# Performance work log

Measured on AMD Instinct MI355X. Metric: run time of the kernel, lower is better.

The kernel has to match this reference:

```python
import jax, jax.numpy as jnp
import numpy as np
from jax import lax

N_SAMPLES = 2 ** 15          # 32768
N_FRAMES = 128
N_HARMONICS = 8
FILT_SIZE = 64
N_EVENTS = 8
N_SCALE = 128                # len(MusicalScale()) assumed = 128 (MIDI notes)
NYQ = 11025.0                # SR22050 nyquist
MIN_F0 = 40.0 / NYQ
MAX_F0 = 3000.0 / NYQ
F0_SPAN = MAX_F0 - MIN_F0
MIN_RES = 0.9
RES_SPAN = 1.0 - MIN_RES
PI = float(np.pi)

# packed layout slices (order of param_sizes dict)
SL_F0 = slice(0, 128)
SL_FINE = slice(128, 256)
SL_AMP = slice(256, 384)
SL_HAMP = slice(384, 392)
SL_HDEC = slice(392, 400)
SL_FENV = slice(400, 464)


def lin_interp(x, out_size):
    """F.interpolate(mode='linear', align_corners=False) along last axis."""
    n = x.shape[-1]
    pos = (jnp.arange(out_size, dtype=x.dtype) + 0.5) * (n / out_size) - 0.5
    pos = jnp.clip(pos, 0.0, n - 1)
    lo = jnp.floor(pos).astype(jnp.int32)
    hi = jnp.minimum(lo + 1, n - 1)
    w = pos - lo.astype(x.dtype)
    return x[..., lo] * (1.0 - w) + x[..., hi] * w


def setup_inputs() -> dict:
    key = jax.random.key(0)
    k1, k2 = jax.random.split(key)
    B = 32 * N_EVENTS  # 256 event rows
    packed = jax.random.normal(k1, (B, 464), dtype=jnp.float32)
    # musical scale: MIDI-note center frequencies normalized by nyquist
    midi = np.arange(N_SCALE)
    freqs = 440.0 * 2.0 ** ((midi - 69) / 12.0) / NYQ
    frequencies = jnp.asarray(freqs, dtype=jnp.float32)
    noise = jax.random.uniform(k2, (B, 1, N_SAMPLES), dtype=jnp.float32)  # mapped to (-1,1) in reference
    return {"packed": packed, "frequencies": frequencies, "noise": noise}


def reference(packed, frequencies, noise):
    B = packed.shape[0]
    p = jax.nn.sigmoid(packed)  # Model applies activation(p) before SynthParams

    # f0: softmax over discrete scale bins, weighted sum of normalized freqs
    f0w = jax.nn.softmax(p[:, SL_F0], axis=-1)             # [B, 128]
    f0 = (f0w @ frequencies)[:, None, None]                # [B,1,1]
    f0 = jnp.broadcast_to(f0, (B, 1, N_FRAMES))            # repeat over frames
    f0 = f0 * NYQ
    f0 = MIN_F0 + f0 * F0_SPAN                             # [B,1,128]
    # NOTE: source computes `f0 + f0 + f0_fine` and discards it -> f0_fine unused

    harmonic_factors = jnp.arange(1, N_HARMONICS + 1, dtype=p.dtype)
    osc = f0 * harmonic_factors[None, :, None]             # [B,8,128]
    radians = osc / NYQ * PI
    radians = lin_interp(radians, N_SAMPLES)               # [B,8,32768]
    osc_bank = jnp.sin(jnp.cumsum(radians, axis=-1))

    harm_decay = MIN_RES + p[:, SL_HDEC] * RES_SPAN        # [B,8]
    harm_amp = p[:, SL_HAMP]                               # [B,8]
    amp = p[:, SL_AMP][:, None, :] * 2.0 - 1.0             # [B,1,128]
    amp_full = lin_interp(amp, N_SAMPLES)                  # [B,1,32768]

    noise_filter = p[:, SL_FENV][:, None, :]               # [B,1,64]
    noise_filter = lin_interp(noise_filter, N_SAMPLES // 2)
    noise_filter = jnp.pad(noise_filter, ((0, 0), (0, 0), (0, 1)))  # [B,1,16385]

    noise_u = noise * 2.0 - 1.0                            # uniform(-1,1)
    noise_spec = jnp.fft.rfft(noise_u, axis=-1, norm='ortho')
    filt = jnp.fft.irfft(noise_spec * noise_filter, n=N_SAMPLES, axis=-1, norm='ortho')
    filt = filt * jnp.clip(amp_full, 0.0, 1.0)             # [B,1,32768]

    # leaky-accumulator recurrence over frames
    def step(cur, a_i):  # cur [B,8], a_i [B]
        cur = jnp.clip(cur + a_i[:, None] * harm_amp, 0.0, 1.0)
        out = cur
        cur = cur * harm_decay
        return cur, out

    amp_t = amp[:, 0, :].T                                 # [128, B]
    _, outs = lax.scan(step, jnp.zeros((B, N_HARMONICS), dtype=p.dtype), amp_t)
    x = jnp.transpose(outs, (1, 2, 0))                     # [B,8,128]
    x = jnp.where(x >= PI, 0.0, x)
    x = lin_interp(x, N_SAMPLES)                           # [B,8,32768]
    x = x * osc_bank
    x = filt + x
    x = x.reshape(-1, N_EVENTS, N_HARMONICS, N_SAMPLES)
    x = jnp.sum(x, axis=(1, 2))[:, None, :]                # [batch,1,32768]
    return x
```

## Files before the change

kernel.cpp:

```cpp
#include <hip/hip_runtime.h>
#include <math.h>

#ifndef M_PI
#define M_PI 3.14159265358979323846
#endif

#define NSAMP 32768
#define MHALF 16384
#define TWO_PI_F 6.2831853071795864f
#define PSTRIDE 1089

__device__ __forceinline__ double dsig(double x) { return 1.0 / (1.0 + exp(-x)); }

__global__ __launch_bounds__(128) void prep_kernel(
    const float* __restrict__ packed, const float* __restrict__ freqs,
    unsigned long long* __restrict__ step, float* __restrict__ env,
    float* __restrict__ amp, float* __restrict__ fenv)
{
    int b = blockIdx.x;
    int t = threadIdx.x;
    const float* pk = packed + b * 464;
    __shared__ double sh_num[128];
    __shared__ double sh_den[128];
    __shared__ double amp_d[128];

    double e_t = exp(dsig((double)pk[t]));
    sh_den[t] = e_t;
    sh_num[t] = e_t * (double)freqs[t];

    double av = dsig((double)pk[256 + t]) * 2.0 - 1.0;
    amp_d[t] = av;
    amp[b * 128 + t] = (float)av;

    if (t < 64) fenv[b * 64 + t] = (float)dsig((double)pk[400 + t]);
    __syncthreads();

    for (int off = 64; off > 0; off >>= 1) {
        if (t < off) { sh_den[t] += sh_den[t + off]; sh_num[t] += sh_num[t + off]; }
        __syncthreads();
    }

    if (t < 8) {
        const double NYQ = 11025.0;
        const double MIN_F0 = 40.0 / NYQ;
        const double MAX_F0 = 3000.0 / NYQ;
        const double F0_SPAN = MAX_F0 - MIN_F0;
        double f0 = sh_num[0] / sh_den[0];
        double F = f0 * NYQ;
        double G = MIN_F0 + F * F0_SPAN;
        double oscf = G * (double)(t + 1);
        double r = oscf / NYQ * M_PI;
        double rv = r / (2.0 * M_PI);
        rv -= floor(rv);
        step[b * 8 + t] = (unsigned long long)(rv * 18446744073709551616.0);

        double ha = dsig((double)pk[384 + t]);
        double hd = 0.9 + dsig((double)pk[392 + t]) * (1.0 - 0.9);
        double cur = 0.0;
        float* eo = env + (size_t)(b * 8 + t) * 128;
        for (int fr = 0; fr < 128; fr++) {
            cur = cur + amp_d[fr] * ha;
            cur = fmin(fmax(cur, 0.0), 1.0);
            eo[fr] = (float)cur;
            cur *= hd;
        }
    }
}

__device__ __forceinline__ float2 cmul(float2 a, float2 b) {
    return make_float2(a.x * b.x - a.y * b.y, a.x * b.y + a.y * b.x);
}

template<int INV>
__device__ __forceinline__ void fft4(float2& x0, float2& x1, float2& x2, float2& x3) {
    float2 s02 = make_float2(x0.x + x2.x, x0.y + x2.y);
    float2 d02 = make_float2(x0.x - x2.x, x0.y - x2.y);
    float2 s13 = make_float2(x1.x + x3.x, x1.y + x3.y);
    float2 d13 = make_float2(x1.x - x3.x, x1.y - x3.y);
    float2 j13 = INV ? make_float2(-d13.y, d13.x) : make_float2(d13.y, -d13.x);
    x0 = make_float2(s02.x + s13.x, s02.y + s13.y);
    x2 = make_float2(s02.x - s13.x, s02.y - s13.y);
    x1 = make_float2(d02.x + j13.x, d02.y + j13.y);
    x3 = make_float2(d02.x - j13.x, d02.y - j13.y);
}

#define V16(v, c) v[((((c) & 3) << 2) | ((c) >> 2))]

template<int INV>
__device__ __forceinline__ void fft16(float2 v[16]) {
    const float s = INV ? 1.0f : -1.0f;
#pragma unroll
    for (int b = 0; b < 4; b++) fft4<INV>(v[b], v[4 + b], v[8 + b], v[12 + b]);
    v[5]  = cmul(v[5],  make_float2(0.9238795325f,  s * 0.3826834324f));
    v[9]  = cmul(v[9],  make_float2(0.7071067812f,  s * 0.7071067812f));
    v[13] = cmul(v[13], make_float2(0.3826834324f,  s * 0.9238795325f));
    v[6]  = cmul(v[6],  make_float2(0.7071067812f,  s * 0.7071067812f));
    v[10] = cmul(v[10], make_float2(0.0f,           s * 1.0f));
    v[14] = cmul(v[14], make_float2(-0.7071067812f, s * 0.7071067812f));
    v[7]  = cmul(v[7],  make_float2(0.3826834324f,  s * 0.9238795325f));
    v[11] = cmul(v[11], make_float2(-0.7071067812f, s * 0.7071067812f));
    v[15] = cmul(v[15], make_float2(-0.9238795325f, s * -0.3826834324f));
#pragma unroll
    for (int p = 0; p < 4; p++) fft4<INV>(v[4 * p], v[4 * p + 1], v[4 * p + 2], v[4 * p + 3]);
}

__device__ __forceinline__ int zaddr(int k) {
    int p = k & 15, k2 = k >> 4;
    int s = 256 * (k2 & 3) + 16 * ((k2 >> 2) & 15) + (k2 >> 6);
    return p * PSTRIDE + s + (s >> 4);
}

__device__ __forceinline__ void plane_fwd(float2* __restrict__ Zp, int l) {
    {
        float sn, cs;
        __sincosf(TWO_PI_F * (float)l * (1.f / 1024.f), &sn, &cs);
        float2 w1 = make_float2(cs, -sn);
        const float2 jstep = make_float2(0.9238795325f, -0.3826834324f);
#pragma unroll
        for (int j = 0; j < 4; j++) {
            const int r = 64 * j + l;
            float2 u0 = Zp[r], u1 = Zp[256 + r], u2 = Zp[512 + r], u3 = Zp[768 + r];
            fft4<0>(u0, u1, u2, u3);
            float2 w2 = cmul(w1, w1);
            float2 w3 = cmul(w2, w1);
            Zp[r] = u0;
            Zp[256 + r] = cmul(u1, w1);
            Zp[512 + r] = cmul(u2, w2);
            Zp[768 + r] = cmul(u3, w3);
            w1 = cmul(w1, jstep);
        }
    }
    {
        const int k4 = l >> 4, c = l & 15;
        const int nbase = 256 * k4 + c;
        float sn, cs;
        __sincosf(TWO_PI_F * (float)c * (1.f / 256.f), &sn, &cs);
        const float2 wc = make_float2(cs, -sn);
        float2 v[16];
#pragma unroll
        for (int b = 0; b < 16; b++) v[b] = Zp[nbase + 16 * b];
        fft16<0>(v);
        const int pbase = 272 * k4 + c;
        Zp[pbase] = V16(v, 0);
        float2 w = wc;
#pragma unroll
        for (int kb = 1; kb < 16; kb++) {
            Zp[pbase + 17 * kb] = cmul(V16(v, kb), w);
            w = cmul(w, wc);
        }
    }
    {
        const int pbase = 272 * (l >> 4) + 17 * (l & 15);
        float2 v[16];
#pragma unroll
        for (int c = 0; c < 16; c++) v[c] = Zp[pbase + c];
        fft16<0>(v);
#pragma unroll
        for (int kc = 0; kc < 16; kc++) Zp[pbase + kc] = V16(v, kc);
    }
}

__device__ __forceinline__ void plane_inv(float2* __restrict__ Zp, int l) {
    {
        const int kb = l & 15;
        const int pbase = 272 * (l >> 4) + 17 * kb;
        float sn, cs;
        __sincosf(TWO_PI_F * (float)kb * (1.f / 256.f), &sn, &cs);
        const float2 wkb = make_float2(cs, sn);
        float2 v[16];
#pragma unroll
        for (int kc = 0; kc < 16; kc++) v[kc] = Zp[pbase + kc];
        fft16<1>(v);
        Zp[pbase] = V16(v, 0);
        float2 w = wkb;
#pragma unroll
        for (int nc = 1; nc < 16; nc++) {
            Zp[pbase + nc] = cmul(V16(v, nc), w);
            w = cmul(w, wkb);
        }
    }
    {
        const int k4 = l >> 4, nc = l & 15;
        const int pbase = 272 * k4 + nc;
        float sni, csi;
        __sincosf(TWO_PI_F * (float)(nc * k4) * (1.f / 1024.f), &sni, &csi);
        float2 t = make_float2(csi, sni);
        float sns, css;
        __sincosf(TWO_PI_F * (float)k4 * (1.f / 64.f), &sns, &css);
        const float2 st = make_float2(css, sns);
        float2 v[16];
#pragma unroll
        for (int kb = 0; kb < 16; kb++) v[kb] = Zp[pbase + 17 * kb];
        fft16<1>(v);
#pragma unroll
        for (int nb = 0; nb < 16; nb++) {
            Zp[pbase + 17 * nb] = cmul(V16(v, nb), t);
            t = cmul(t, st);
        }
    }
#pragma unroll
    for (int j = 0; j < 4; j++) {
        const int r = 64 * j + l;
        const int rp = r + (r >> 4);
        float2 u0 = Zp[rp], u1 = Zp[272 + rp], u2 = Zp[544 + rp], u3 = Zp[816 + rp];
        fft4<1>(u0, u1, u2, u3);
        Zp[rp] = u0; Zp[272 + rp] = u1; Zp[544 + rp] = u2; Zp[816 + rp] = u3;
    }
}

__device__ __forceinline__ float hinterp64(const float* f, int j) {
    float pos = ((float)j + 0.5f) * (1.0f / 256.0f) - 0.5f;
    pos = fminf(fmaxf(pos, 0.0f), 63.0f);
    int lo = (int)pos;
    int hi = min(lo + 1, 63);
    float w = pos - (float)lo;
    return f[lo] * (1.0f - w) + f[hi] * w;
}

__global__ __launch_bounds__(1024, 4) void fft_kernel(
    const float* __restrict__ noise, const float* __restrict__ amp,
    const float* __restrict__ fenv, float* __restrict__ filt)
{
    __shared__ float2 Z[16 * PSTRIDE];
    __shared__ float fenv_s[64];
    __shared__ float amp_s[128];
    const int bb = blockIdx.x;
    const int tid = threadIdx.x;
    const int wv = tid >> 6, l = tid & 63;

    if (tid < 64) fenv_s[tid] = fenv[bb * 64 + tid];
    if (tid < 128) amp_s[tid] = amp[bb * 128 + tid];

    const float2* nz = (const float2*)(noise + (size_t)bb * NSAMP);

    {
        float2 v[16];
#pragma unroll
        for (int a = 0; a < 16; a++) {
            float2 t = nz[a * 1024 + tid];
            v[a] = make_float2(t.x * 2.f - 1.f, t.y * 2.f - 1.f);
        }
        fft16<0>(v);
        float sn, cs;
        __sincosf(TWO_PI_F * (float)tid * (1.f / 16384.f), &sn, &cs);
        const float2 ws = make_float2(cs, -sn);
        Z[tid] = V16(v, 0);
        float2 w = ws;
#pragma unroll
        for (int k1 = 1; k1 < 16; k1++) {
            Z[k1 * PSTRIDE + tid] = cmul(V16(v, k1), w);
            w = cmul(w, ws);
        }
    }
    __syncthreads();

    plane_fwd(Z + wv * PSTRIDE, l);
    __syncthreads();

    const float invM = 1.0f / (float)MHALF;
    {
        float sn0, cs0;
        __sincosf((float)M_PI * (float)tid * (1.f / 16384.f), &sn0, &cs0);
        float2 t = make_float2(cs0, sn0);
        const float2 tstep = make_float2(0.98078528040323f, 0.19509032201613f);
        for (int k = tid; k <= 8192; k += 1024) {
            if (k == 0) {
                int i0 = zaddr(0);
                float2 Z0 = Z[i0];
                float Y0 = (Z0.x + Z0.y) * hinterp64(fenv_s, 0);
                float vv = Y0 * 0.5f * invM;
                Z[i0] = make_float2(vv, vv);
            } else if (k == 8192) {
                int i8 = zaddr(8192);
                float s = hinterp64(fenv_s, 8192) * invM;
                float2 Zk = Z[i8];
                Z[i8] = make_float2(Zk.x * s, Zk.y * s);
            } else {
                int ik = zaddr(k), imk = zaddr(16384 - k);
                float2 Zk = Z[ik], Zm = Z[imk];
                float Ex = 0.5f * (Zk.x + Zm.x);
                float Ey = 0.5f * (Zk.y - Zm.y);
                float Ox = 0.5f * (Zk.y + Zm.y);
                float Oy = -0.5f * (Zk.x - Zm.x);
                float cs = t.x, sn = t.y;
                float Xkx = Ex + cs * Ox + sn * Oy;
                float Xky = Ey + cs * Oy - sn * Ox;
                float Xmx = Ex - cs * Ox - sn * Oy;
                float Xmy = -Ey + cs * Oy - sn * Ox;
                float Hk = hinterp64(fenv_s, k);
                float Hm = hinterp64(fenv_s, 16384 - k);
                float Ykx = Xkx * Hk, Yky = Xky * Hk;
                float Ymx = Xmx * Hm, Ymy = Xmy * Hm;
                float Er = 0.5f * (Ykx + Ymx);
                float Ei = 0.5f * (Yky - Ymy);
                float Pr = 0.5f * (Ykx - Ymx);
                float Pi = 0.5f * (Yky + Ymy);
                float Oyx = Pr * cs - Pi * sn;
                float Oyy = Pr * sn + Pi * cs;
                Z[ik]  = make_float2((Er - Oyy) * invM, (Ei + Oyx) * invM);
                Z[imk] = make_float2((Er + Oyy) * invM, (-Ei + Oyx) * invM);
            }
            t = cmul(t, tstep);
        }
    }
    __syncthreads();

    plane_inv(Z + wv * PSTRIDE, l);
    __syncthreads();

    {
        const int tp = tid + (tid >> 4);
        float2 v[16];
#pragma unroll
        for (int k1 = 0; k1 < 16; k1++) v[k1] = Z[k1 * PSTRIDE + tp];
        float sn, cs;
        __sincosf(TWO_PI_F * (float)tid * (1.f / 16384.f), &sn, &cs);
        const float2 wg = make_float2(cs, sn);
        float2 w = wg;
#pragma unroll
        for (int k1 = 1; k1 < 16; k1++) {
            v[k1] = cmul(v[k1], w);
            w = cmul(w, wg);
        }
        fft16<1>(v);

        float2* fo = (float2*)(filt + (size_t)bb * NSAMP);
#pragma unroll
        for (int m = 0; m < 16; m++) {
            float2 y = V16(v, m);
            int A = m * 1024 + tid;
            int s0 = 2 * A;
            float p0 = ((float)s0 + 0.5f) * (1.0f / 256.0f) - 0.5f;
            float p1 = p0 + (1.0f / 256.0f);
            p0 = fminf(fmaxf(p0, 0.0f), 127.0f);
            p1 = fminf(fmaxf(p1, 0.0f), 127.0f);
            int l0 = (int)p0, l1 = (int)p1;
            int h0 = min(l0 + 1, 127), h1 = min(l1 + 1, 127);
            float w0a = p0 - (float)l0, w1a = p1 - (float)l1;
            float a0 = amp_s[l0] * (1.0f - w0a) + amp_s[h0] * w0a;
            float a1 = amp_s[l1] * (1.0f - w1a) + amp_s[h1] * w1a;
            a0 = fminf(fmaxf(a0, 0.0f), 1.0f);
            a1 = fminf(fmaxf(a1, 0.0f), 1.0f);
            fo[A] = make_float2(y.x * a0, y.y * a1);
        }
    }
}

__global__ __launch_bounds__(256) void synth_kernel(
    const unsigned long long* __restrict__ step, const float* __restrict__ env,
    const float* __restrict__ filt, float* __restrict__ out)
{
    const int chunk = blockIdx.x;
    const int g = blockIdx.y;
    const int tid = threadIdx.x;
    __shared__ float env_s[64 * 128];
    __shared__ unsigned long long step_s[64];

    const float* eg = env + (size_t)g * 64 * 128;
    for (int i = tid; i < 64 * 128; i += 256) env_s[i] = eg[i];
    if (tid < 64) step_s[tid] = step[g * 64 + tid];
    __syncthreads();

    const int s0 = chunk * 1024 + tid * 4;

    float4 aF = make_float4(0.f, 0.f, 0.f, 0.f);
#pragma unroll
    for (int e = 0; e < 8; e++) {
        const float4 f = *(const float4*)(filt + ((size_t)(g * 8 + e)) * NSAMP + s0);
        aF.x += f.x; aF.y += f.y; aF.z += f.z; aF.w += f.w;
    }

    float c0v[4], c1v[4], c2v[4];
    int lo0;
    {
        float pos0 = ((float)s0 + 0.5f) * (1.0f / 256.0f) - 0.5f;
        pos0 = fminf(fmaxf(pos0, 0.0f), 127.0f);
        lo0 = (int)pos0;
#pragma unroll
        for (int k = 0; k < 4; k++) {
            float pos = ((float)(s0 + k) + 0.5f) * (1.0f / 256.0f) - 0.5f;
            pos = fminf(fmaxf(pos, 0.0f), 127.0f);
            int lo = (int)pos;
            float w = pos - (float)lo;
            if (lo == lo0) { c0v[k] = 1.0f - w; c1v[k] = w;        c2v[k] = 0.0f; }
            else           { c0v[k] = 0.0f;     c1v[k] = 1.0f - w; c2v[k] = w;    }
        }
    }
    const int i1 = min(lo0 + 1, 127);
    int lo3b = lo0;
    {
        float pos = ((float)(s0 + 3) + 0.5f) * (1.0f / 256.0f) - 0.5f;
        pos = fminf(fmaxf(pos, 0.0f), 127.0f);
        lo3b = (int)pos;
    }
    const int i2 = min(lo3b + 1, 127);

    float a0 = 0.f, a1 = 0.f, a2 = 0.f, a3 = 0.f;
    const unsigned long long n0 = (unsigned long long)(unsigned)(s0 + 1);

#pragma unroll 8
    for (int idx = 0; idx < 64; idx++) {
        const unsigned long long st = step_s[idx];
        unsigned long long p = st * n0;
        const float* er = env_s + (idx << 7);
        const float v0 = er[lo0], v1 = er[i1], v2 = er[i2];

        float ev, fr, sn;

        fr = (float)(unsigned)(p >> 32) * 0x1p-32f;
        sn = __builtin_amdgcn_sinf(fr);
        ev = fmaf(v0, c0v[0], fmaf(v1, c1v[0], v2 * c2v[0]));
        a0 = fmaf(ev, sn, a0); p += st;

        fr = (float)(unsigned)(p >> 32) * 0x1p-32f;
        sn = __builtin_amdgcn_sinf(fr);
        ev = fmaf(v0, c0v[1], fmaf(v1, c1v[1], v2 * c2v[1]));
        a1 = fmaf(ev, sn, a1); p += st;

        fr = (float)(unsigned)(p >> 32) * 0x1p-32f;
        sn = __builtin_amdgcn_sinf(fr);
        ev = fmaf(v0, c0v[2], fmaf(v1, c1v[2], v2 * c2v[2]));
        a2 = fmaf(ev, sn, a2); p += st;

        fr = (float)(unsigned)(p >> 32) * 0x1p-32f;
        sn = __builtin_amdgcn_sinf(fr);
        ev = fmaf(v0, c0v[3], fmaf(v1, c1v[3], v2 * c2v[3]));
        a3 = fmaf(ev, sn, a3);
    }

    float4 r;
    r.x = a0 + 8.0f * aF.x;
    r.y = a1 + 8.0f * aF.y;
    r.z = a2 + 8.0f * aF.z;
    r.w = a3 + 8.0f * aF.w;
    *(float4*)(out + (size_t)g * NSAMP + s0) = r;
}

extern "C" void kernel_launch(void* const* d_in, const int* in_sizes, int n_in,
                              void* d_out, int out_size, void* d_ws, size_t ws_size,
                              hipStream_t stream)
{
    (void)in_sizes; (void)n_in; (void)out_size; (void)ws_size;
    const float* packed = (const float*)d_in[0];
    const float* freqs  = (const float*)d_in[1];
    const float* noise  = (const float*)d_in[2];
    float* out = (float*)d_out;
    char* ws = (char*)d_ws;

    unsigned long long* step = (unsigned long long*)(ws);
    float* env  = (float*)(ws + 16384);
    float* amp  = (float*)(ws + 16384 + 1048576);
    float* fenv = (float*)(ws + 16384 + 1048576 + 131072);
    float* filt = (float*)(ws + 16384 + 1048576 + 131072 + 65536);

    hipLaunchKernelGGL(prep_kernel, dim3(256), dim3(128), 0, stream,
                       packed, freqs, step, env, amp, fenv);
    hipLaunchKernelGGL(fft_kernel, dim3(256), dim3(1024), 0, stream,
                       noise, amp, fenv, filt);
    hipLaunchKernelGGL(synth_kernel, dim3(32, 32), dim3(256), 0, stream,
                       step, env, filt, out);
}
```

Measured before the change: 144.1 us.

## Fuse parameter prep into FFT kernel and use incremental float phase in synth

```diff
diff --git a/kernel.cpp b/kernel.cpp
--- a/kernel.cpp
+++ b/kernel.cpp
@@ -11,61 +11,6 @@
 #define PSTRIDE 1089
 
 __device__ __forceinline__ double dsig(double x) { return 1.0 / (1.0 + exp(-x)); }
-
-__global__ __launch_bounds__(128) void prep_kernel(
-    const float* __restrict__ packed, const float* __restrict__ freqs,
-    unsigned long long* __restrict__ step, float* __restrict__ env,
-    float* __restrict__ amp, float* __restrict__ fenv)
-{
-    int b = blockIdx.x;
-    int t = threadIdx.x;
-    const float* pk = packed + b * 464;
-    __shared__ double sh_num[128];
-    __shared__ double sh_den[128];
-    __shared__ double amp_d[128];
-
-    double e_t = exp(dsig((double)pk[t]));
-    sh_den[t] = e_t;
-    sh_num[t] = e_t * (double)freqs[t];
-
-    double av = dsig((double)pk[256 + t]) * 2.0 - 1.0;
-    amp_d[t] = av;
-    amp[b * 128 + t] = (float)av;
-
-    if (t < 64) fenv[b * 64 + t] = (float)dsig((double)pk[400 + t]);
-    __syncthreads();
-
-    for (int off = 64; off > 0; off >>= 1) {
-        if (t < off) { sh_den[t] += sh_den[t + off]; sh_num[t] += sh_num[t + off]; }
-        __syncthreads();
-    }
-
-    if (t < 8) {
-        const double NYQ = 11025.0;
-        const double MIN_F0 = 40.0 / NYQ;
-        const double MAX_F0 = 3000.0 / NYQ;
-        const double F0_SPAN = MAX_F0 - MIN_F0;
-        double f0 = sh_num[0] / sh_den[0];
-        double F = f0 * NYQ;
-        double G = MIN_F0 + F * F0_SPAN;
-        double oscf = G * (double)(t + 1);
-        double r = oscf / NYQ * M_PI;
-        double rv = r / (2.0 * M_PI);
-        rv -= floor(rv);
-        step[b * 8 + t] = (unsigned long long)(rv * 18446744073709551616.0);
-
-        double ha = dsig((double)pk[384 + t]);
-        double hd = 0.9 + dsig((double)pk[392 + t]) * (1.0 - 0.9);
-        double cur = 0.0;
-        float* eo = env + (size_t)(b * 8 + t) * 128;
-        for (int fr = 0; fr < 128; fr++) {
-            cur = cur + amp_d[fr] * ha;
-            cur = fmin(fmax(cur, 0.0), 1.0);
-            eo[fr] = (float)cur;
-            cur *= hd;
-        }
-    }
-}
 
 __device__ __forceinline__ float2 cmul(float2 a, float2 b) {
     return make_float2(a.x * b.x - a.y * b.y, a.x * b.y + a.y * b.x);
@@ -218,18 +163,65 @@
 }
 
 __global__ __launch_bounds__(1024, 4) void fft_kernel(
-    const float* __restrict__ noise, const float* __restrict__ amp,
-    const float* __restrict__ fenv, float* __restrict__ filt)
+    const float* __restrict__ packed, const float* __restrict__ freqs,
+    const float* __restrict__ noise,
+    unsigned long long* __restrict__ step, float* __restrict__ env,
+    float* __restrict__ filt)
 {
     __shared__ float2 Z[16 * PSTRIDE];
     __shared__ float fenv_s[64];
     __shared__ float amp_s[128];
+    __shared__ double ampd_s[128];
     const int bb = blockIdx.x;
     const int tid = threadIdx.x;
     const int wv = tid >> 6, l = tid & 63;
 
-    if (tid < 64) fenv_s[tid] = fenv[bb * 64 + tid];
-    if (tid < 128) amp_s[tid] = amp[bb * 128 + tid];
+    if (tid < 64) {
+        const float* pk = packed + bb * 464;
+        double e0 = exp(dsig((double)pk[tid]));
+        double e1 = exp(dsig((double)pk[tid + 64]));
+        double num = e0 * (double)freqs[tid] + e1 * (double)freqs[tid + 64];
+        double den = e0 + e1;
+#pragma unroll
+        for (int off = 32; off > 0; off >>= 1) {
+            num += __shfl_down(num, off);
+            den += __shfl_down(den, off);
+        }
+        num = __shfl(num, 0);
+        den = __shfl(den, 0);
+
+        double a0 = dsig((double)pk[256 + tid]) * 2.0 - 1.0;
+        double a1 = dsig((double)pk[256 + 64 + tid]) * 2.0 - 1.0;
+        ampd_s[tid] = a0; ampd_s[tid + 64] = a1;
+        amp_s[tid] = (float)a0; amp_s[tid + 64] = (float)a1;
+        fenv_s[tid] = (float)dsig((double)pk[400 + tid]);
+
+        if (tid < 8) {
+            const double NYQ = 11025.0;
+            const double MIN_F0 = 40.0 / NYQ;
+            const double MAX_F0 = 3000.0 / NYQ;
+            const double F0_SPAN = MAX_F0 - MIN_F0;
+            double f0 = num / den;
+            double F = f0 * NYQ;
+            double G = MIN_F0 + F * F0_SPAN;
+            double oscf = G * (double)(tid + 1);
+            double r = oscf / NYQ * M_PI;
+            double rv = r / (2.0 * M_PI);
+            rv -= floor(rv);
+            step[bb * 8 + tid] = (unsigned long long)(rv * 18446744073709551616.0);
+
+            double ha = dsig((double)pk[384 + tid]);
+            double hd = 0.9 + dsig((double)pk[392 + tid]) * (1.0 - 0.9);
+            double cur = 0.0;
+            float* eo = env + (size_t)(bb * 8 + tid) * 128;
+            for (int fr = 0; fr < 128; fr++) {
+                cur = cur + ampd_s[fr] * ha;
+                cur = fmin(fmax(cur, 0.0), 1.0);
+                eo[fr] = (float)cur;
+                cur *= hd;
+            }
+        }
+    }
 
     const float2* nz = (const float2*)(noise + (size_t)bb * NSAMP);
 
@@ -401,28 +393,29 @@
 #pragma unroll 8
     for (int idx = 0; idx < 64; idx++) {
         const unsigned long long st = step_s[idx];
-        unsigned long long p = st * n0;
+        const unsigned long long p = st * n0;
+        const float stf = (float)(unsigned)(st >> 32) * 0x1p-32f;
+        float fr = (float)(unsigned)(p >> 32) * 0x1p-32f;
         const float* er = env_s + (idx << 7);
         const float v0 = er[lo0], v1 = er[i1], v2 = er[i2];
 
-        float ev, fr, sn;
-
-        fr = (float)(unsigned)(p >> 32) * 0x1p-32f;
+        float ev, sn;
+
         sn = __builtin_amdgcn_sinf(fr);
         ev = fmaf(v0, c0v[0], fmaf(v1, c1v[0], v2 * c2v[0]));
-        a0 = fmaf(ev, sn, a0); p += st;
-
-        fr = (float)(unsigned)(p >> 32) * 0x1p-32f;
+        a0 = fmaf(ev, sn, a0);
+        fr = __builtin_amdgcn_fractf(fr + stf);
+
         sn = __builtin_amdgcn_sinf(fr);
         ev = fmaf(v0, c0v[1], fmaf(v1, c1v[1], v2 * c2v[1]));
-        a1 = fmaf(ev, sn, a1); p += st;
-
-        fr = (float)(unsigned)(p >> 32) * 0x1p-32f;
+        a1 = fmaf(ev, sn, a1);
+        fr = __builtin_amdgcn_fractf(fr + stf);
+
         sn = __builtin_amdgcn_sinf(fr);
         ev = fmaf(v0, c0v[2], fmaf(v1, c1v[2], v2 * c2v[2]));
-        a2 = fmaf(ev, sn, a2); p += st;
-
-        fr = (float)(unsigned)(p >> 32) * 0x1p-32f;
+        a2 = fmaf(ev, sn, a2);
+        fr = __builtin_amdgcn_fractf(fr + stf);
+
         sn = __builtin_amdgcn_sinf(fr);
         ev = fmaf(v0, c0v[3], fmaf(v1, c1v[3], v2 * c2v[3]));
         a3 = fmaf(ev, sn, a3);
@@ -449,14 +442,10 @@
 
     unsigned long long* step = (unsigned long long*)(ws);
     float* env  = (float*)(ws + 16384);
-    float* amp  = (float*)(ws + 16384 + 1048576);
-    float* fenv = (float*)(ws + 16384 + 1048576 + 131072);
     float* filt = (float*)(ws + 16384 + 1048576 + 131072 + 65536);
 
-    hipLaunchKernelGGL(prep_kernel, dim3(256), dim3(128), 0, stream,
-                       packed, freqs, step, env, amp, fenv);
     hipLaunchKernelGGL(fft_kernel, dim3(256), dim3(1024), 0, stream,
-                       noise, amp, fenv, filt);
+                       packed, freqs, noise, step, env, filt);
     hipLaunchKernelGGL(synth_kernel, dim3(32, 32), dim3(256), 0, stream,
                        step, env, filt, out);
 }
```

Result: faster. 134.6 us (-6.6%).
